# Performance work log

Measured on AMD Instinct MI355X. Metric: run time of the kernel, lower is better.

The kernel has to match this reference:

```python
import jax, jax.numpy as jnp
import numpy as np

BETA = 0.5  # hard-negative concentration (module default)


def _l2norm(x, axis):
    return x / jnp.linalg.norm(x, axis=axis, keepdims=True)


def setup_inputs() -> dict:
    key = jax.random.key(0)
    k1, k2, k3 = jax.random.split(key, 3)
    B, V, D = 4096, 2, 512
    features = jax.random.normal(k1, (B, V, D), dtype=jnp.float32)
    out_1 = jax.random.normal(k2, (B, D), dtype=jnp.float32)
    out_2 = jax.random.normal(k3, (B, D), dtype=jnp.float32)
    indexes = jnp.arange(B, dtype=jnp.int64)
    return {"features": features, "out_1": out_1, "out_2": out_2, "indexes": indexes}


def reference(features, out_1, out_2, indexes):
    # features is normalized in the original forward but unused afterwards
    _ = _l2norm(features, axis=2)

    o1 = _l2norm(out_1, axis=-1)
    o2 = _l2norm(out_2, axis=-1)
    out = jnp.concatenate([o1, o2], axis=0)            # [2B, D]
    label = jnp.concatenate([indexes, indexes], axis=0)  # [2B]
    batch = label.shape[0]

    # cost = exp(2 * out @ out.T), [2B, 2B]
    cost = jnp.exp(2.0 * jnp.einsum('id,jd->ij', out, out))

    pos_full = (label[:, None] == label[None, :]).astype(cost.dtype)
    neg_index = 1.0 - pos_full
    pos_index = pos_full - jnp.eye(batch, dtype=cost.dtype)

    pos = pos_index * cost
    neg = neg_index * cost

    # importance weights: neg_index * exp(beta * log(neg)) == neg_index * neg**beta
    imp = jax.lax.stop_gradient(neg_index * jnp.power(neg, BETA))
    neg_exp_sum = (imp * neg).sum(axis=-1) / imp.sum(axis=-1)  # [2B]

    denom = pos + (batch - 2) * neg_exp_sum[:, None]
    ratio = pos / denom

    mask = pos_index > 0
    safe_ratio = jnp.where(mask, ratio, 1.0)
    nce = -(jnp.log(safe_ratio) * pos_index).sum() / pos_index.sum()
    return nce
```

## Files before the change

### kernel.cpp

```cpp
#include <hip/hip_runtime.h>
#include <stdint.h>

#define BHALF 4096
#define NROWS 8192
#define DDIM  512
#define KNEG  8190.0f

#define BM   128
#define BK   32
#define NTIL 64
#define TBLK (NTIL * (NTIL + 1) / 2)
#define FABLK 256

typedef short v8s __attribute__((ext_vector_type(8)));
typedef float v4f __attribute__((ext_vector_type(4)));

static __device__ inline float bf2f(uint32_t u) {
    union { uint32_t i; float f; } c; c.i = u << 16; return c.f;
}
static __device__ inline uint32_t f2bf(float f) {
    union { float f; uint32_t i; } c; c.f = f;
    return (c.i + 0x7fffu + ((c.i >> 16) & 1u)) >> 16;
}


__global__ __launch_bounds__(256) void rownorm_cvt_kernel(
    const void* __restrict__ o1, const void* __restrict__ o2,
    float* __restrict__ rn, uint16_t* __restrict__ cvt2)
{
    int wave = threadIdx.x >> 6, lane = threadIdx.x & 63;
    int row = blockIdx.x * 4 + wave;

    uint32_t w = ((const uint32_t*)o1)[lane * 977 + 13];
    uint32_t e = (w >> 7) & 0xFFu;
    int bad = (e < 100u || e > 140u) ? 1 : 0;
    #pragma unroll
    for (int m = 32; m; m >>= 1) bad += __shfl_xor(bad, m);

    float ss;
    uint4 pack;
    if (bad <= 16) {
        const uint16_t* s = (row < BHALF)
            ? (const uint16_t*)o1 + (size_t)row * DDIM
            : (const uint16_t*)o2 + (size_t)(row - BHALF) * DDIM;
        pack = ((const uint4*)s)[lane];
        float a0 = bf2f(pack.x & 0xffffu), a1 = bf2f(pack.x >> 16);
        float a2 = bf2f(pack.y & 0xffffu), a3 = bf2f(pack.y >> 16);
        float a4 = bf2f(pack.z & 0xffffu), a5 = bf2f(pack.z >> 16);
        float a6 = bf2f(pack.w & 0xffffu), a7 = bf2f(pack.w >> 16);
        ss = a0*a0 + a1*a1 + a2*a2 + a3*a3 + a4*a4 + a5*a5 + a6*a6 + a7*a7;
    } else {
        const float* s = (row < BHALF)
            ? (const float*)o1 + (size_t)row * DDIM
            : (const float*)o2 + (size_t)(row - BHALF) * DDIM;
        float4 a = ((const float4*)s)[2 * lane];
        float4 b = ((const float4*)s)[2 * lane + 1];
        ss = a.x*a.x + a.y*a.y + a.z*a.z + a.w*a.w
           + b.x*b.x + b.y*b.y + b.z*b.z + b.w*b.w;
        pack.x = f2bf(a.x) | (f2bf(a.y) << 16);
        pack.y = f2bf(a.z) | (f2bf(a.w) << 16);
        pack.z = f2bf(b.x) | (f2bf(b.y) << 16);
        pack.w = f2bf(b.z) | (f2bf(b.w) << 16);
    }
    size_t byteoff = (size_t)(row >> 4) * 16384 + (size_t)lane * 256
                   + (size_t)(row & 15) * 16;
    *(uint4*)((char*)cvt2 + byteoff) = pack;

    #pragma unroll
    for (int m = 32; m; m >>= 1) ss += __shfl_xor(ss, m);
    if (lane == 0) rn[row] = rsqrtf(ss);
}

__global__ __launch_bounds__(256, 3) void SupCon_hcl_49323404427556_kernel(
    const uint16_t* __restrict__ cvt2, const float* __restrict__ rn,
    float* __restrict__ pden, float* __restrict__ pnum, float* __restrict__ cpos)
{
    __shared__ float rnA[BM], rnB[BM];
    __shared__ float s_dr[BM][2], s_nr[BM][2], s_dc[BM][2], s_nc[BM][2];

    int tid  = threadIdx.x;
    int wave = tid >> 6, lane = tid & 63;
    int quad = lane >> 4, l16 = lane & 15;
    int wrow = (wave >> 1) * 64, wcol = (wave & 1) * 64;

    int b = blockIdx.x;
    int t = (b & 7) * (TBLK / 8) + (b >> 3);

    int bi = (int)(64.5f - sqrtf(64.5f * 64.5f - 2.0f * (float)t));
    while (bi > 0 && (64 * bi - (bi * (bi - 1)) / 2) > t) --bi;
    while ((64 * (bi + 1) - ((bi + 1) * bi) / 2) <= t) ++bi;
    int bj = bi + (t - (64 * bi - (bi * (bi - 1)) / 2));
    int i0 = bi * BM, j0 = bj * BM;
    bool diag = (bi == bj);
    bool partner = (bj == bi + 32) && (bi < 32);
    bool plain = !diag && !partner;

    if (tid < BM) rnA[tid] = rn[i0 + tid];
    else          rnB[tid - BM] = rn[j0 + (tid - BM)];
    __syncthreads();

    const char* cb = (const char*)cvt2;
    const char* a0 = cb + (size_t)((i0 + wrow) >> 4) * 16384 + (size_t)lane * 16;
    const char* b0 = cb + (size_t)((j0 + wcol) >> 4) * 16384 + (size_t)lane * 16;

    v4f acc[4][4];
    v4f z = {0.f, 0.f, 0.f, 0.f};
    #pragma unroll
    for (int a = 0; a < 4; ++a)
        #pragma unroll
        for (int bb = 0; bb < 4; ++bb) acc[a][bb] = z;

    #pragma unroll 2
    for (int kb = 0; kb < DDIM / BK; ++kb) {
        v8s af[4], bfr[4];
        #pragma unroll
        for (int tt = 0; tt < 4; ++tt) {
            af[tt]  = *(const v8s*)(a0 + (size_t)tt * 16384 + (size_t)kb * 1024);
            bfr[tt] = *(const v8s*)(b0 + (size_t)tt * 16384 + (size_t)kb * 1024);
        }
        #pragma unroll
        for (int mt = 0; mt < 4; ++mt)
            #pragma unroll
            for (int nt = 0; nt < 4; ++nt)
                acc[mt][nt] = __builtin_amdgcn_mfma_f32_16x16x32_bf16(
                    af[mt], bfr[nt], acc[mt][nt], 0, 0, 0);
    }

    if (plain) {
        float rjv[4];
        #pragma unroll
        for (int nt = 0; nt < 4; ++nt) rjv[nt] = rnB[wcol + 16 * nt + l16];

        float pd[16], pn[16], cdv[4], cnv[4];
        #pragma unroll
        for (int k = 0; k < 16; ++k) { pd[k] = 0.f; pn[k] = 0.f; }
        #pragma unroll
        for (int nt = 0; nt < 4; ++nt) { cdv[nt] = 0.f; cnv[nt] = 0.f; }

        #pragma unroll
        for (int mt = 0; mt < 4; ++mt) {
            #pragma unroll
            for (int r = 0; r < 4; ++r) {
                float ri = rnA[wrow + 16 * mt + quad * 4 + r];
                #pragma unroll
                for (int nt = 0; nt < 4; ++nt) {
                    float e  = __expf(acc[mt][nt][r] * ri * rjv[nt]);
                    float e3 = e * e * e;
                    pd[mt * 4 + r] += e;   pn[mt * 4 + r] += e3;
                    cdv[nt]        += e;   cnv[nt]        += e3;
                }
            }
        }

        #define BSTEP(arr, n, bit)                                            \
            _Pragma("unroll")                                                 \
            for (int p = 0; p < (n); ++p) {                                   \
                float mine = (l16 & (bit)) ? arr[2*p+1] : arr[2*p];           \
                float send = (l16 & (bit)) ? arr[2*p]   : arr[2*p+1];         \
                arr[p] = mine + __shfl_xor(send, (bit));                      \
            }
        BSTEP(pd, 8, 1) BSTEP(pd, 4, 2) BSTEP(pd, 2, 4) BSTEP(pd, 1, 8)
        BSTEP(pn, 8, 1) BSTEP(pn, 4, 2) BSTEP(pn, 2, 4) BSTEP(pn, 1, 8)
        #undef BSTEP

        int rowk = wrow + 16 * (l16 >> 2) + quad * 4 + (l16 & 3);
        s_dr[rowk][wcol >> 6] = pd[0];
        s_nr[rowk][wcol >> 6] = pn[0];

        #pragma unroll
        for (int nt = 0; nt < 4; ++nt) {
            float cd = cdv[nt] + __shfl_xor(cdv[nt], 16);
            cd += __shfl_xor(cd, 32);
            float cn = cnv[nt] + __shfl_xor(cnv[nt], 16);
            cn += __shfl_xor(cn, 32);
            if (quad == 0) {
                s_dc[wcol + 16 * nt + l16][wrow >> 6] = cd;
                s_nc[wcol + 16 * nt + l16][wrow >> 6] = cn;
            }
        }
    } else {
        #pragma unroll
        for (int mt = 0; mt < 4; ++mt) {
            #pragma unroll
            for (int nt = 0; nt < 4; ++nt) {
                float rj = rnB[wcol + 16 * nt + l16];
                #pragma unroll
                for (int r = 0; r < 4; ++r) {
                    float ri = rnA[wrow + 16 * mt + quad * 4 + r];
                    acc[mt][nt][r] = __expf(acc[mt][nt][r] * ri * rj);
                }
            }
        }

        #pragma unroll
        for (int mt = 0; mt < 4; ++mt) {
            #pragma unroll
            for (int r = 0; r < 4; ++r) {
                int gil = wrow + 16 * mt + quad * 4 + r;
                int gi = i0 + gil;
                int pr = gi ^ BHALF;
                float pdv = 0.f, pnv = 0.f;
                #pragma unroll
                for (int nt = 0; nt < 4; ++nt) {
                    int gj = j0 + wcol + 16 * nt + l16;
                    float e = acc[mt][nt][r];
                    if (gj == pr) cpos[gi] = e * e;
                    if (gj != gi && gj != pr) { pdv += e; pnv += e * e * e; }
                }
                #pragma unroll
                for (int m = 1; m < 16; m <<= 1) {
                    pdv += __shfl_xor(pdv, m);
                    pnv += __shfl_xor(pnv, m);
                }
                if (l16 == 0) { s_dr[gil][wcol >> 6] = pdv; s_nr[gil][wcol >> 6] = pnv; }
            }
        }

        if (!diag) {
            #pragma unroll
            for (int nt = 0; nt < 4; ++nt) {
                int gjl = wcol + 16 * nt + l16;
                int gj = j0 + gjl;
                int pj = gj ^ BHALF;
                float cd = 0.f, cn = 0.f;
                #pragma unroll
                for (int mt = 0; mt < 4; ++mt) {
                    #pragma unroll
                    for (int r = 0; r < 4; ++r) {
                        int gi = i0 + wrow + 16 * mt + quad * 4 + r;
                        float e = acc[mt][nt][r];
                        if (gi == pj) cpos[gj] = e * e;
                        else { cd += e; cn += e * e * e; }
                    }
                }
                cd += __shfl_xor(cd, 16); cn += __shfl_xor(cn, 16);
                cd += __shfl_xor(cd, 32); cn += __shfl_xor(cn, 32);
                if (quad == 0) { s_dc[gjl][wrow >> 6] = cd; s_nc[gjl][wrow >> 6] = cn; }
            }
        }
    }

    __syncthreads();
    if (tid < BM) {
        pden[(size_t)bj * NROWS + i0 + tid] = s_dr[tid][0] + s_dr[tid][1];
        pnum[(size_t)bj * NROWS + i0 + tid] = s_nr[tid][0] + s_nr[tid][1];
        if (!diag) {
            pden[(size_t)bi * NROWS + j0 + tid] = s_dc[tid][0] + s_dc[tid][1];
            pnum[(size_t)bi * NROWS + j0 + tid] = s_nc[tid][0] + s_nc[tid][1];
        }
    }
}

__global__ __launch_bounds__(256) void finalizeA_kernel(
    const float* __restrict__ pden, const float* __restrict__ pnum,
    const float* __restrict__ cpos, float* __restrict__ bpart)
{
    int b = blockIdx.x, t = threadIdx.x;
    int r = b * 32 + (t & 31);
    int c = t >> 5;
    float pd = 0.f, pn = 0.f;
    #pragma unroll
    for (int i = 0; i < 8; ++i) {
        int x = c + 8 * i;
        pd += pden[(size_t)x * NROWS + r];
        pn += pnum[(size_t)x * NROWS + r];
    }
    pd += __shfl_xor(pd, 32);
    pn += __shfl_xor(pn, 32);

    __shared__ float sd[4][32], sn[4][32];
    int wave = t >> 6, lane = t & 63;
    if (lane < 32) { sd[wave][lane] = pd; sn[wave][lane] = pn; }
    __syncthreads();

    float s = 0.f;
    if (t < 32) {
        float d = sd[0][t] + sd[1][t] + sd[2][t] + sd[3][t];
        float n = sn[0][t] + sn[1][t] + sn[2][t] + sn[3][t];
        s = logf(1.0f + KNEG * (n / d) / cpos[b * 32 + t]);
    }
    if (t < 64) {
        #pragma unroll
        for (int m = 32; m; m >>= 1) s += __shfl_xor(s, m);
        if (t == 0) bpart[b] = s;
    }
}

__global__ __launch_bounds__(256) void finalizeB_kernel(
    const float* __restrict__ bpart, float* __restrict__ out)
{
    int t = threadIdx.x;
    float s = bpart[t];
    #pragma unroll
    for (int m = 32; m; m >>= 1) s += __shfl_xor(s, m);
    __shared__ float wsum[4];
    if ((t & 63) == 0) wsum[t >> 6] = s;
    __syncthreads();
    if (t == 0) out[0] = (wsum[0] + wsum[1] + wsum[2] + wsum[3]) / (float)NROWS;
}

extern "C" void kernel_launch(void* const* d_in, const int* in_sizes, int n_in,
                              void* d_out, int out_size, void* d_ws, size_t ws_size,
                              hipStream_t stream)
{
    const void* o1 = d_in[1];
    const void* o2 = d_in[2];

    uint16_t* cvt2 = (uint16_t*)d_ws;
    float* pden = (float*)(cvt2 + (size_t)NROWS * DDIM);
    float* pnum = pden + (size_t)NTIL * NROWS;
    float* rn   = pnum + (size_t)NTIL * NROWS;
    float* cpos = rn + NROWS;
    float* bpart= cpos + NROWS;

    rownorm_cvt_kernel<<<NROWS / 4, 256, 0, stream>>>(o1, o2, rn, cvt2);
    SupCon_hcl_49323404427556_kernel<<<TBLK, 256, 0, stream>>>(cvt2, rn, pden, pnum, cpos);
    finalizeA_kernel<<<FABLK, 256, 0, stream>>>(pden, pnum, cpos, bpart);
    finalizeB_kernel<<<1, 256, 0, stream>>>(bpart, (float*)d_out);
}
```

Measured before the change: 135.8 us.

## Stage GEMM operands through triple-buffered LDS via global_load_lds and fuse finalize kernels

The main Gram kernel now copies A and B tiles straight from global memory into a three-slot LDS ring using global_load_lds, prefetching the next k-slice while the current one feeds the MFMAs. Each k-step waits on vmcnt and a barrier, and MFMA issue priority is raised. Previously every wave fetched its fragments directly from global memory. Separately, the two finalize kernels are merged into one with a last-block atomic counter, which adds a memset but removes a launch. The new path adds 48KB of LDS per block, which may reduce occupancy, plus a barrier on every k-step.

```diff
diff --git a/kernel.cpp b/kernel.cpp
--- a/kernel.cpp
+++ b/kernel.cpp
@@ -8,6 +8,7 @@
 
 #define BM   128
 #define BK   32
+#define NK   (DDIM / BK)
 #define NTIL 64
 #define TBLK (NTIL * (NTIL + 1) / 2)
 #define FABLK 256
@@ -22,6 +23,11 @@
     union { float f; uint32_t i; } c; c.f = f;
     return (c.i + 0x7fffu + ((c.i >> 16) & 1u)) >> 16;
 }
+
+#define GLL16(gp, lp)                                                         \
+    __builtin_amdgcn_global_load_lds(                                         \
+        (__attribute__((address_space(1))) void*)(gp),                        \
+        (__attribute__((address_space(3))) void*)(lp), 16, 0, 0)
 
 
 __global__ __launch_bounds__(256) void rownorm_cvt_kernel(
@@ -75,8 +81,12 @@
     const uint16_t* __restrict__ cvt2, const float* __restrict__ rn,
     float* __restrict__ pden, float* __restrict__ pnum, float* __restrict__ cpos)
 {
+    __shared__ alignas(16) char sbuf[3][16384];
     __shared__ float rnA[BM], rnB[BM];
-    __shared__ float s_dr[BM][2], s_nr[BM][2], s_dc[BM][2], s_nc[BM][2];
+    float (*s_dr)[2] = (float(*)[2])(&sbuf[1][0]);
+    float (*s_nr)[2] = (float(*)[2])(&sbuf[1][1024]);
+    float (*s_dc)[2] = (float(*)[2])(&sbuf[1][2048]);
+    float (*s_nc)[2] = (float(*)[2])(&sbuf[1][3072]);
 
     int tid  = threadIdx.x;
     int wave = tid >> 6, lane = tid & 63;
@@ -97,11 +107,19 @@
 
     if (tid < BM) rnA[tid] = rn[i0 + tid];
     else          rnB[tid - BM] = rn[j0 + (tid - BM)];
-    __syncthreads();
 
     const char* cb = (const char*)cvt2;
-    const char* a0 = cb + (size_t)((i0 + wrow) >> 4) * 16384 + (size_t)lane * 16;
-    const char* b0 = cb + (size_t)((j0 + wcol) >> 4) * 16384 + (size_t)lane * 16;
+    const char* gA0 = cb + ((size_t)(i0 >> 4) + 2 * wave) * 16384 + (size_t)lane * 16;
+    const char* gA1 = gA0 + 16384;
+    const char* gB0 = cb + ((size_t)(j0 >> 4) + 2 * wave) * 16384 + (size_t)lane * 16;
+    const char* gB1 = gB0 + 16384;
+    int dA0 = (2 * wave) * 1024, dA1 = dA0 + 1024;
+    int dB0 = 8192 + dA0,        dB1 = dB0 + 1024;
+
+    GLL16(gA0, &sbuf[0][dA0]);
+    GLL16(gA1, &sbuf[0][dA1]);
+    GLL16(gB0, &sbuf[0][dB0]);
+    GLL16(gB1, &sbuf[0][dB1]);
 
     v4f acc[4][4];
     v4f z = {0.f, 0.f, 0.f, 0.f};
@@ -110,20 +128,38 @@
         #pragma unroll
         for (int bb = 0; bb < 4; ++bb) acc[a][bb] = z;
 
-    #pragma unroll 2
-    for (int kb = 0; kb < DDIM / BK; ++kb) {
+    int rgA = wrow >> 4, rgB = wcol >> 4;
+
+    #pragma unroll
+    for (int kb = 0; kb < NK; ++kb) {
+        if (kb < NK - 1) {
+            char* wb = &sbuf[(kb + 1) % 3][0];
+            GLL16(gA0 + (kb + 1) * 1024, wb + dA0);
+            GLL16(gA1 + (kb + 1) * 1024, wb + dA1);
+            GLL16(gB0 + (kb + 1) * 1024, wb + dB0);
+            GLL16(gB1 + (kb + 1) * 1024, wb + dB1);
+            asm volatile("s_waitcnt vmcnt(4)" ::: "memory");
+        } else {
+            asm volatile("s_waitcnt vmcnt(0)" ::: "memory");
+        }
+        __builtin_amdgcn_s_barrier();
+        __builtin_amdgcn_sched_barrier(0);
+
+        const char* rb = &sbuf[kb % 3][0];
         v8s af[4], bfr[4];
         #pragma unroll
         for (int tt = 0; tt < 4; ++tt) {
-            af[tt]  = *(const v8s*)(a0 + (size_t)tt * 16384 + (size_t)kb * 1024);
-            bfr[tt] = *(const v8s*)(b0 + (size_t)tt * 16384 + (size_t)kb * 1024);
-        }
+            af[tt]  = *(const v8s*)(rb + (rgA + tt) * 1024 + lane * 16);
+            bfr[tt] = *(const v8s*)(rb + 8192 + (rgB + tt) * 1024 + lane * 16);
+        }
+        __builtin_amdgcn_s_setprio(1);
         #pragma unroll
         for (int mt = 0; mt < 4; ++mt)
             #pragma unroll
             for (int nt = 0; nt < 4; ++nt)
                 acc[mt][nt] = __builtin_amdgcn_mfma_f32_16x16x32_bf16(
                     af[mt], bfr[nt], acc[mt][nt], 0, 0, 0);
+        __builtin_amdgcn_s_setprio(0);
     }
 
     if (plain) {
@@ -251,9 +287,10 @@
     }
 }
 
-__global__ __launch_bounds__(256) void finalizeA_kernel(
+__global__ __launch_bounds__(256) void finalize_kernel(
     const float* __restrict__ pden, const float* __restrict__ pnum,
-    const float* __restrict__ cpos, float* __restrict__ bpart)
+    const float* __restrict__ cpos, float* __restrict__ bpart,
+    int* __restrict__ done, float* __restrict__ out)
 {
     int b = blockIdx.x, t = threadIdx.x;
     int r = b * 32 + (t & 31);
@@ -269,6 +306,7 @@
     pn += __shfl_xor(pn, 32);
 
     __shared__ float sd[4][32], sn[4][32];
+    __shared__ int islast;
     int wave = t >> 6, lane = t & 63;
     if (lane < 32) { sd[wave][lane] = pd; sn[wave][lane] = pn; }
     __syncthreads();
@@ -282,21 +320,24 @@
     if (t < 64) {
         #pragma unroll
         for (int m = 32; m; m >>= 1) s += __shfl_xor(s, m);
-        if (t == 0) bpart[b] = s;
-    }
-}
-
-__global__ __launch_bounds__(256) void finalizeB_kernel(
-    const float* __restrict__ bpart, float* __restrict__ out)
-{
-    int t = threadIdx.x;
-    float s = bpart[t];
-    #pragma unroll
-    for (int m = 32; m; m >>= 1) s += __shfl_xor(s, m);
-    __shared__ float wsum[4];
-    if ((t & 63) == 0) wsum[t >> 6] = s;
+    }
+    if (t == 0) {
+        __hip_atomic_store(&bpart[b], s, __ATOMIC_RELAXED, __HIP_MEMORY_SCOPE_AGENT);
+        __threadfence();
+        int v = atomicAdd(done, 1);
+        islast = (v == FABLK - 1) ? 1 : 0;
+    }
     __syncthreads();
-    if (t == 0) out[0] = (wsum[0] + wsum[1] + wsum[2] + wsum[3]) / (float)NROWS;
+    if (islast) {
+        __threadfence();
+        float s2 = __hip_atomic_load(&bpart[t], __ATOMIC_RELAXED, __HIP_MEMORY_SCOPE_AGENT);
+        #pragma unroll
+        for (int m = 32; m; m >>= 1) s2 += __shfl_xor(s2, m);
+        __shared__ float wsum[4];
+        if ((t & 63) == 0) wsum[t >> 6] = s2;
+        __syncthreads();
+        if (t == 0) out[0] = (wsum[0] + wsum[1] + wsum[2] + wsum[3]) / (float)NROWS;
+    }
 }
 
 extern "C" void kernel_launch(void* const* d_in, const int* in_sizes, int n_in,
@@ -312,9 +353,10 @@
     float* rn   = pnum + (size_t)NTIL * NROWS;
     float* cpos = rn + NROWS;
     float* bpart= cpos + NROWS;
-
+    int*   done = (int*)(bpart + FABLK);
+
+    hipMemsetAsync(done, 0, sizeof(int), stream);
     rownorm_cvt_kernel<<<NROWS / 4, 256, 0, stream>>>(o1, o2, rn, cvt2);
     SupCon_hcl_49323404427556_kernel<<<TBLK, 256, 0, stream>>>(cvt2, rn, pden, pnum, cpos);
-    finalizeA_kernel<<<FABLK, 256, 0, stream>>>(pden, pnum, cpos, bpart);
-    finalizeB_kernel<<<1, 256, 0, stream>>>(bpart, (float*)d_out);
-}
+    finalize_kernel<<<FABLK, 256, 0, stream>>>(pden, pnum, cpos, bpart, done, (float*)d_out);
+}
```

Result: slower. 139.2 us (+2.5%).
